# Kernel tuning notes

Measured on AMD Instinct MI355X. Metric: run time of the kernel, lower is better.

The kernel has to match this reference:

```python
import jax, jax.numpy as jnp
import numpy as np

STAGE_SHAPES = {
    'stage1': [(12, 10, 3, 3), (12, 12, 3, 3), (12, 12, 3, 3)],
    'stage2': [(24, 22, 3, 3), (24, 24, 3, 3), (12, 24, 3, 3)],
    'stage3': [(24, 22, 3, 3), (24, 24, 3, 3), (12, 24, 3, 3)],
    'stage4': [(11, 22, 1, 1)],
}
BN_CH = [12, 12, 12, 24, 24, 12, 24, 24, 12]  # channels of the 9 BN layers, in forward order
OFF = np.concatenate([[0], np.cumsum(BN_CH)]).tolist()
EPS = 1e-5


def _split_weights(wflat, shapes):
    """Slice flat [B, P] hypernet weights into per-layer [B, O, I, k, k] tensors."""
    outs, bg = [], 0
    for s in shapes:
        n = int(np.prod(s))
        outs.append(wflat[:, bg:bg + n].reshape((-1,) + s))
        bg += n
    return outs


def _per_sample_conv(x, w):
    """x: [B, C, H, W], w: [B, O, C, k, k] -> [B, O, H, W]. Each sample uses its own filters (SAME padding = k//2 for odd k)."""
    def one(xi, wi):
        return jax.lax.conv_general_dilated(
            xi[None], wi, window_strides=(1, 1), padding='SAME',
            dimension_numbers=('NCHW', 'OIHW', 'NCHW'))[0]
    return jax.vmap(one)(x, w)


def _bn_eval(y, gamma, beta, mean, var):
    """Eval-mode BatchNorm2d over channel dim of [B, C, H, W]."""
    inv = gamma * jax.lax.rsqrt(var + EPS)
    return y * inv[None, :, None, None] + (beta - mean * inv)[None, :, None, None]


def setup_inputs():
    key = jax.random.key(0)
    ks = jax.random.split(key, 8)
    B, H, W = 64, 128, 128
    x = jax.random.normal(ks[0], (B, 10, H, W), jnp.float32)
    # scale hypernet weights down so 9 stacked convs stay numerically tame
    w_stage1 = jax.random.normal(ks[1], (B, 3672), jnp.float32) * 0.05
    w_stage2 = jax.random.normal(ks[2], (B, 12528), jnp.float32) * 0.05
    w_stage3 = jax.random.normal(ks[3], (B, 12528), jnp.float32) * 0.05
    w_stage4 = jax.random.normal(ks[4], (B, 242), jnp.float32) * 0.05
    n_bn = sum(BN_CH)  # 144
    bn_gamma = jax.random.uniform(ks[5], (n_bn,), jnp.float32, 0.5, 1.5)
    bn_beta = jax.random.normal(ks[6], (n_bn,), jnp.float32) * 0.1
    bn_mean = jnp.zeros((n_bn,), jnp.float32)
    bn_var = jnp.ones((n_bn,), jnp.float32)
    return dict(x=x, w_stage1=w_stage1, w_stage2=w_stage2, w_stage3=w_stage3,
                w_stage4=w_stage4, bn_gamma=bn_gamma, bn_beta=bn_beta,
                bn_mean=bn_mean, bn_var=bn_var)


def reference(x, w_stage1, w_stage2, w_stage3, w_stage4, bn_gamma, bn_beta, bn_mean, bn_var):
    cur = x
    li = 0  # global BN layer index
    for stage_key, wflat in (('stage1', w_stage1), ('stage2', w_stage2), ('stage3', w_stage3)):
        for w in _split_weights(wflat, STAGE_SHAPES[stage_key]):
            conv = _per_sample_conv(cur, w)
            lo, hi = OFF[li], OFF[li + 1]
            bn = _bn_eval(conv, bn_gamma[lo:hi], bn_beta[lo:hi], bn_mean[lo:hi], bn_var[lo:hi])
            cur = jax.nn.relu(bn)
            li += 1
        cur = jnp.concatenate([cur, x], axis=1)  # dense skip: [B, 12+10, H, W]
    w_pred = _split_weights(w_stage4, STAGE_SHAPES['stage4'])[0]  # [B, 11, 22, 1, 1]
    return _per_sample_conv(cur, w_pred)
```

## Files before the change

kernel.cpp:

```cpp
#include <hip/hip_runtime.h>
#include <stdint.h>

#define HW    16384
#define NB    64
#define W2    130
#define PXS   (W2*W2)
#define WQH   70144
#define EPSB  1e-5f
#define GP    1444
#define GPB   23104
#define ROWB  608
#define ZPB   2560

typedef _Float16 h8  __attribute__((ext_vector_type(8)));
typedef _Float16 h4  __attribute__((ext_vector_type(4)));
typedef float    f16v __attribute__((ext_vector_type(16)));
typedef float    f4  __attribute__((ext_vector_type(4)));
typedef h8 uh8 __attribute__((aligned(4)));
typedef h4 uh4 __attribute__((aligned(4)));
typedef f4 uf4 __attribute__((aligned(4)));

__global__ void prep_w(const float* __restrict__ w1, const float* __restrict__ w2,
                       const float* __restrict__ w3, const float* __restrict__ w4,
                       const float* __restrict__ g,  const float* __restrict__ be,
                       const float* __restrict__ mu, const float* __restrict__ va,
                       _Float16* __restrict__ wq, float* __restrict__ bias)
{
    const int FO[11]   = {0,576,1152,1728,2880,4032,5184,6336,7488,8640,8768};
    const int start[10]= {0,1080,2376,3672,8424,13608,16200,20952,26136,28728};
    const int COt[10]  = {12,12,12,24,24,12,24,24,12,11};
    const int CIt[10]  = {10,12,12,22,24,24,22,24,24,22};
    const int bnoff[10]= {0,12,24,36,60,84,96,120,144,0};
    const int KST[10]  = {1,1,1,2,2,2,2,2,2,2};

    long tid = (long)blockIdx.x * 256 + threadIdx.x;
    long total = (long)NB * 8768, stride = (long)gridDim.x * 256;
    for (long idx = tid; idx < total; idx += stride) {
        int b = (int)(idx / 8768), i = (int)(idx - (long)b * 8768);
        int l = 9; while (i < FO[l]) --l;
        int j = i - FO[l];
        int f = j >> 6, lane = j & 63;
        int ks = (KST[l] == 2) ? (f & 1) : 0;
        int s  = (KST[l] == 2) ? (f >> 1) : f;
        int co = lane & 31, hi = lane >> 5;
        int CO = COt[l], CI = CIt[l];
        float scale = 1.f;
        if (l < 9 && co < CO) {
            int bi = bnoff[l] + co;
            scale = g[bi] * rsqrtf(va[bi] + EPSB);
        }
        int c0 = ks * 16 + hi * 8;
        __attribute__((aligned(16))) _Float16 vals[8];
#pragma unroll
        for (int e = 0; e < 8; ++e) {
            int c = c0 + e; float wv = 0.f;
            if (co < CO && c < CI) {
                int p = (l < 9) ? start[l] + (co * CI + c) * 9 + s
                                : start[9] + co * CI + c;
                const float* src; long si;
                if      (p <  3672) { src = w1; si = (long)b *  3672 + p; }
                else if (p < 16200) { src = w2; si = (long)b * 12528 + (p -  3672); }
                else if (p < 28728) { src = w3; si = (long)b * 12528 + (p - 16200); }
                else                { src = w4; si = (long)b *   242 + (p - 28728); }
                wv = src[si] * scale;
            }
            vals[e] = (_Float16)wv;
        }
        *(uh8*)(wq + idx * 8) = *(const h8*)vals;
    }
    if (tid < 320) {
        int l = (int)tid >> 5, co = (int)tid & 31;
        float v = 0.f;
        if (l < 9 && co < COt[l]) {
            int bi = bnoff[l] + co;
            float sc = g[bi] * rsqrtf(va[bi] + EPSB);
            v = be[bi] - mu[bi] * sc;
        }
        bias[tid] = v;
    }
}

__global__ void pad_x(const float* __restrict__ x, _Float16* __restrict__ bufA,
                      _Float16* __restrict__ bufB, int b0)
{
    int sl = blockIdx.x >> 3, part = blockIdx.x & 7;
    int gb = b0 + sl;
    const float* __restrict__ xs = x + (long)gb * 10 * HW;
    _Float16* __restrict__ dA = bufA + (long)sl * PXS * 32;
    _Float16* __restrict__ dB = bufB + (long)sl * PXS * 32;
    for (int p = part * 256 + threadIdx.x; p < PXS; p += 2048) {
        int r = p / W2, cc = p - r * W2;
        __attribute__((aligned(16))) _Float16 pxA[32], pxB[32];
#pragma unroll
        for (int i = 0; i < 32; ++i) { pxA[i] = (_Float16)0.f; pxB[i] = (_Float16)0.f; }
        if (r >= 1 && r <= 128 && cc >= 1 && cc <= 128) {
            int so = (r - 1) * 128 + (cc - 1);
#pragma unroll
            for (int c = 0; c < 10; ++c) {
                _Float16 xv = (_Float16)xs[c * HW + so];
                pxA[c] = xv; pxA[12 + c] = xv; pxB[12 + c] = xv;
            }
        }
        _Float16* ap = dA + (long)p * 32;
        _Float16* bp = dB + (long)p * 32;
#pragma unroll
        for (int q = 0; q < 4; ++q) {
            *(uh8*)(ap + q * 8) = *(const h8*)(pxA + q * 8);
            *(uh8*)(bp + q * 8) = *(const h8*)(pxB + q * 8);
        }
    }
}

template<int KST, int NR, int TNWV, bool REV>
__device__ __forceinline__ void lconv(const char* pin, char* pout,
    const char* zbase,
    const _Float16* wl, const float* __restrict__ bias, int boff,
    int rowStart, int nRows, int colStart, int width,
    int oy0, int ox0, int w, int lo5, int hi)
{
    constexpr int qmax = (KST == 1) ? 2 : 3;
    constexpr int NG = 3 * KST;
    constexpr int FR = 9 * KST;

    h8 afr[FR];
#pragma unroll
    for (int f = 0; f < FR; ++f) afr[f] = *(const uh8*)(wl + (long)f * 512);

    const int ncb = (width > 32) ? 2 : 1;
    const int nrg = (nRows + NR - 1) / NR;
    const int nu  = nrg * ncb;
#pragma unroll 1
    for (int u = w; u < nu; u += TNWV) {
        int rg, cb;
        if (ncb == 2) { rg = u >> 1; cb = u & 1; } else { rg = u; cb = 0; }
        int r0 = rowStart + rg * NR;
        { int rmax = rowStart + nRows - NR; r0 = (r0 > rmax) ? rmax : r0; }
        const int cs   = cb ? (colStart + width - 32) : colStart;
        const int cmin = cb ? (64 - width) : 0;
        const char* bin = pin + (long)hi * GPB
                        + ((long)(r0 - 1) * 38 + (cs - 1 + lo5)) * 16;
        const char* binH = bin + 2 * GPB;
        if (KST == 2 && hi) binH = zbase;

        f16v acc[NR];
        { f16v z = {};
#pragma unroll
          for (int i = 0; i < NR; ++i) acc[i] = z; }

#pragma unroll
        for (int gg = 0; gg < NG; ++gg) {
            const int g  = REV ? (NG - 1 - gg) : gg;
            const int kc = g / KST, ks = g - kc * KST;
            const char* base = ks ? binH : bin;
            h8 bf[NR + 2];
#pragma unroll
            for (int j = 0; j < NR + 2; ++j)
                bf[j] = *(const uh8*)(base + kc * 16 + j * ROWB);
            __builtin_amdgcn_s_setprio(1);
#pragma unroll
            for (int kr = 0; kr < 3; ++kr)
#pragma unroll
                for (int tt = 0; tt < NR; ++tt)
                    acc[tt] = __builtin_amdgcn_mfma_f32_32x32x16_f16(
                                  afr[(kr * 3 + kc) * KST + ks], bf[kr + tt], acc[tt], 0, 0, 0);
            __builtin_amdgcn_s_setprio(0);
        }

        f4 bv[qmax];
#pragma unroll
        for (int q = 0; q < qmax; ++q) bv[q] = *(const uf4*)(bias + boff + hi * 4 + q * 8);
        const bool cok = (lo5 >= cmin);
        const int  pc  = cs + lo5;
        const int  gx  = ox0 - 3 + pc;
        const bool xin = (unsigned)(gx - 1) < 128u;
        char* pob = pout + (long)hi * 8 + ((long)r0 * 38 + pc) * 16;
        if (cok) {
#pragma unroll
            for (int tt = 0; tt < NR; ++tt) {
                int gy = oy0 - 3 + r0 + tt;
                bool ok = xin && ((unsigned)(gy - 1) < 128u);
#pragma unroll
                for (int q = 0; q < qmax; ++q) {
                    float v0 = ok ? fmaxf(acc[tt][4*q+0] + bv[q][0], 0.f) : 0.f;
                    float v1 = ok ? fmaxf(acc[tt][4*q+1] + bv[q][1], 0.f) : 0.f;
                    float v2 = ok ? fmaxf(acc[tt][4*q+2] + bv[q][2], 0.f) : 0.f;
                    float v3 = ok ? fmaxf(acc[tt][4*q+3] + bv[q][3], 0.f) : 0.f;
                    h4 hv = { (_Float16)v0, (_Float16)v1, (_Float16)v2, (_Float16)v3 };
                    *(uh4*)(pob + q * GPB + tt * ROWB) = hv;
                }
            }
        }
    }
}

template<int KST, int TNTH>
__global__ __launch_bounds__(TNTH)
void stage3(const _Float16* __restrict__ in, _Float16* __restrict__ out,
            const _Float16* __restrict__ wq, int loff0,
            const float* __restrict__ bias, int boff0, int b0)
{
    constexpr int NGR  = (KST == 1) ? 2 : 3;
    constexpr int PLHk = NGR * GP * 8;
    constexpr int TNWV = TNTH / 64;
    __shared__ _Float16 lds[2][PLHk];
    __shared__ char zpad[(KST == 2) ? ZPB : 16];

    const int t = threadIdx.x, w = t >> 6, l = t & 63;
    const int lo5 = l & 31, hi = l >> 5;

    const int nbb = (int)(gridDim.x >> 4);
    int s, tile;
    if ((nbb & 7) == 0) {
        int xcd = (int)(blockIdx.x & 7), j = (int)(blockIdx.x >> 3);
        s = xcd * (nbb >> 3) + (j >> 4); tile = j & 15;
    } else { s = (int)(blockIdx.x >> 4); tile = (int)(blockIdx.x & 15); }
    const int gb  = b0 + s;
    const int oy0 = 1 + (tile >> 2) * 32;
    const int ox0 = 1 + (tile & 3) * 32;

    {
        constexpr int NLD = NGR * GP;
        constexpr int SI  = (NLD + TNTH - 1) / TNTH;
        const char* src = (const char*)(in + (long)s * PXS * 32);
        char* dst = (char*)&lds[0][0];
        h8 stg[SI];
#pragma unroll
        for (int k = 0; k < SI; ++k) {
            int idx = k * TNTH + t;
            int p = idx / NGR, c = idx - p * NGR;
            int r = p / 38, cc = p - r * 38;
            int gy = oy0 - 3 + r, gx = ox0 - 3 + cc;
            h8 v = {};
            if (idx < NLD && (unsigned)gy < 130u && (unsigned)gx < 130u)
                v = *(const uh8*)(src + ((long)gy * W2 + gx) * 64 + c * 16);
            stg[k] = v;
        }
#pragma unroll
        for (int k = 0; k < SI; ++k) {
            int idx = k * TNTH + t;
            int p = idx / NGR, c = idx - p * NGR;
            if (idx < NLD)
                *(uh8*)(dst + (long)c * GPB + (long)p * 16) = stg[k];
        }
        if (KST == 2 && t < ZPB / 16) {
            h8 z = {};
            *(uh8*)(zpad + t * 16) = z;
        }
    }
    __syncthreads();

    const _Float16* wl = wq + (long)gb * WQH + loff0 + (long)l * 8;
    const char* zb = (const char*)zpad;
    constexpr int LSTEP = 9 * KST * 512;
#define LCONV(PIN, POUT, WOFF, BOFF, RS, NRW, CS, WD)                          \
    if (w & 1) lconv<KST,3,TNWV,true >((const char*)(PIN), (char*)(POUT), zb,  \
        wl + (WOFF), bias, boff0 + (BOFF), RS, NRW, CS, WD, oy0, ox0, w, lo5, hi); \
    else       lconv<KST,3,TNWV,false>((const char*)(PIN), (char*)(POUT), zb,  \
        wl + (WOFF), bias, boff0 + (BOFF), RS, NRW, CS, WD, oy0, ox0, w, lo5, hi);

    LCONV(lds[0], lds[1], 0,         0,  1, 36, 1, 36);
    __syncthreads();
    LCONV(lds[1], lds[0], LSTEP,     32, 2, 34, 2, 34);
    __syncthreads();
    LCONV(lds[0], lds[1], 2 * LSTEP, 64, 3, 32, 3, 32);
    __syncthreads();
#undef LCONV

    {
        _Float16* db = out + (long)s * PXS * 32;
        const char* T = (const char*)&lds[1][0];
        constexpr int WB = (1024 + TNTH - 1) / TNTH;
#pragma unroll
        for (int k = 0; k < WB; ++k) {
            int px = k * TNTH + t;
            if (px < 1024) {
                int pr = 3 + (px >> 5), pc = 3 + (px & 31);
                int gy = oy0 + (px >> 5), gx = ox0 + (px & 31);
                const char* sp = T + ((long)pr * 38 + pc) * 16;
                h8 v0 = *(const uh8*)sp;
                h4 v1 = *(const uh4*)(sp + GPB);
                _Float16* dp = db + ((long)gy * W2 + gx) * 32;
                *(uh8*)dp = v0;
                *(uh4*)(dp + 8) = v1;
            }
        }
    }
}

__global__ __launch_bounds__(256, 2)
void conv1(const _Float16* __restrict__ in, float* __restrict__ outF,
           const _Float16* __restrict__ wq, int loff, int b0)
{
    const int s = blockIdx.y, gb = b0 + s;
    const int t = threadIdx.x, w = t >> 6, l = t & 63;
    const int lo5 = l & 31, hi = l >> 5;
    const int cb = blockIdx.x & 3;
    const int y00 = (blockIdx.x >> 2) * 32 + w * 8;
    const int xpix = cb * 32 + lo5;

    const _Float16* wl = wq + (long)gb * WQH + loff + (long)l * 8;
    h8 a0 = *(const uh8*)(wl);
    h8 a1 = *(const uh8*)(wl + 512);
    const _Float16* ib = in + (long)s * PXS * 32;

#pragma unroll 1
    for (int tt = 0; tt < 8; ++tt) {
        int y = y00 + tt;
        const _Float16* bp = ib + ((long)(y + 1) * W2 + xpix + 1) * 32 + hi * 8;
        h8 bA = *(const uh8*)(bp);
        h8 bB = *(const uh8*)(bp + 16);
        f16v acc = {};
        acc = __builtin_amdgcn_mfma_f32_32x32x16_f16(a0, bA, acc, 0, 0, 0);
        acc = __builtin_amdgcn_mfma_f32_32x32x16_f16(a1, bB, acc, 0, 0, 0);
        long px = (long)y * 128 + xpix;
#pragma unroll
        for (int r = 0; r < 16; ++r) {
            int co = (r & 3) + 8 * (r >> 2) + 4 * hi;
            if (co < 11) outF[((long)gb * 11 + co) * HW + px] = acc[r];
        }
    }
}

extern "C" void kernel_launch(void* const* d_in, const int* in_sizes, int n_in,
                              void* d_out, int out_size, void* d_ws, size_t ws_size,
                              hipStream_t stream)
{
    const float *x = (const float*)d_in[0], *w1 = (const float*)d_in[1],
                *w2 = (const float*)d_in[2], *w3 = (const float*)d_in[3],
                *w4 = (const float*)d_in[4], *g  = (const float*)d_in[5],
                *be = (const float*)d_in[6], *mu = (const float*)d_in[7],
                *va = (const float*)d_in[8];
    if (n_in == 9) {
        const float* big801[2] = {nullptr, nullptr}; int n801 = 0;
        const float* bn156[4]  = {nullptr, nullptr, nullptr, nullptr}; int n156 = 0;
        const float *fx = nullptr, *fw1 = nullptr, *fw4 = nullptr;
        for (int i = 0; i < 9; ++i) {
            int sz = in_sizes[i];
            if      (sz == 10485760) fx  = (const float*)d_in[i];
            else if (sz ==   235008) fw1 = (const float*)d_in[i];
            else if (sz ==   801792) { if (n801 < 2) big801[n801++] = (const float*)d_in[i]; }
            else if (sz ==    15488) fw4 = (const float*)d_in[i];
            else if (sz ==      156) { if (n156 < 4) bn156[n156++] = (const float*)d_in[i]; }
        }
        if (fx && fw1 && fw4 && n801 == 2 && n156 == 4) {
            x = fx; w1 = fw1; w2 = big801[0]; w3 = big801[1]; w4 = fw4;
            g = bn156[0]; be = bn156[1]; mu = bn156[2]; va = bn156[3];
        }
    }
    float* out = (float*)d_out;

    const size_t wqB   = (size_t)NB * WQH * 2;
    const size_t biasB = 2048;
    const size_t hdr   = wqB + biasB;
    const size_t perSlot = (size_t)PXS * 128;
    size_t avail = ws_size > hdr ? ws_size - hdr : 0;
    int chunk = (int)(avail / perSlot);
    if (chunk > NB) chunk = NB;
    if (chunk < 1)  chunk = 1;

    _Float16* wq   = (_Float16*)d_ws;
    float*    bias = (float*)((char*)d_ws + wqB);
    _Float16* bufA = (_Float16*)((char*)d_ws + hdr);
    _Float16* bufB = bufA + (size_t)chunk * PXS * 32;

    prep_w<<<2048, 256, 0, stream>>>(w1, w2, w3, w4, g, be, mu, va, wq, bias);

    for (int b0 = 0; b0 < NB; b0 += chunk) {
        int nb = (NB - b0 < chunk) ? (NB - b0) : chunk;
        pad_x<<<nb * 8, 256, 0, stream>>>(x, bufA, bufB, b0);
        int gc = nb * 16;
        dim3 g1(16, nb);
        stage3<1,1024><<<gc, 1024, 0, stream>>>(bufA, bufB, wq,     0, bias,   0, b0);
        stage3<2, 768><<<gc,  768, 0, stream>>>(bufB, bufA, wq, 13824, bias,  96, b0);
        stage3<2, 768><<<gc,  768, 0, stream>>>(bufA, bufB, wq, 41472, bias, 192, b0);
        conv1<<<g1, 256, 0, stream>>>(bufB, out, wq, 69120, b0);
    }
}
```

Measured before the change: 461.1 us.

## Reshape fused-stage tiles from 32x32 to 16x64 and drop reversed-order waves

Changes the per-block output tile of the fused three-conv stage kernel from 32x32 to 16 rows by 64 columns, widening the LDS halo layout to 22x70 and generalising column blocking to any number of 32-wide chunks. The wider tile lowers the halo overhead in the column direction, which suits the 32-wide MFMA column blocks, at the cost of more row halo. It also removes the reversed tap-group ordering for odd waves, which had been meant to stagger LDS access across waves. LDS footprint per block grows slightly, which may affect occupancy.

```diff
diff --git a/kernel.cpp b/kernel.cpp
--- a/kernel.cpp
+++ b/kernel.cpp
@@ -7,10 +7,12 @@
 #define PXS   (W2*W2)
 #define WQH   70144
 #define EPSB  1e-5f
-#define GP    1444
-#define GPB   23104
-#define ROWB  608
-#define ZPB   2560
+#define WCOL  70
+#define WROW  22
+#define GP    (WROW*WCOL)
+#define GPB   (GP*16)
+#define ROWB  (WCOL*16)
+#define ZPB   4608
 
 typedef _Float16 h8  __attribute__((ext_vector_type(8)));
 typedef _Float16 h4  __attribute__((ext_vector_type(4)));
@@ -111,7 +113,7 @@
     }
 }
 
-template<int KST, int NR, int TNWV, bool REV>
+template<int KST, int NR, int TNWV>
 __device__ __forceinline__ void lconv(const char* pin, char* pout,
     const char* zbase,
     const _Float16* wl, const float* __restrict__ bias, int boff,
@@ -126,19 +128,19 @@
 #pragma unroll
     for (int f = 0; f < FR; ++f) afr[f] = *(const uh8*)(wl + (long)f * 512);
 
-    const int ncb = (width > 32) ? 2 : 1;
+    const int ncb = (width + 31) >> 5;
     const int nrg = (nRows + NR - 1) / NR;
     const int nu  = nrg * ncb;
 #pragma unroll 1
     for (int u = w; u < nu; u += TNWV) {
-        int rg, cb;
-        if (ncb == 2) { rg = u >> 1; cb = u & 1; } else { rg = u; cb = 0; }
+        const int rg = u / ncb, cb = u - rg * ncb;
         int r0 = rowStart + rg * NR;
         { int rmax = rowStart + nRows - NR; r0 = (r0 > rmax) ? rmax : r0; }
-        const int cs   = cb ? (colStart + width - 32) : colStart;
-        const int cmin = cb ? (64 - width) : 0;
+        const bool last = (cb == ncb - 1);
+        const int cs   = last ? (colStart + width - 32) : (colStart + cb * 32);
+        const int cmin = last ? (ncb * 32 - width) : 0;
         const char* bin = pin + (long)hi * GPB
-                        + ((long)(r0 - 1) * 38 + (cs - 1 + lo5)) * 16;
+                        + ((long)(r0 - 1) * WCOL + (cs - 1 + lo5)) * 16;
         const char* binH = bin + 2 * GPB;
         if (KST == 2 && hi) binH = zbase;
 
@@ -148,8 +150,7 @@
           for (int i = 0; i < NR; ++i) acc[i] = z; }
 
 #pragma unroll
-        for (int gg = 0; gg < NG; ++gg) {
-            const int g  = REV ? (NG - 1 - gg) : gg;
+        for (int g = 0; g < NG; ++g) {
             const int kc = g / KST, ks = g - kc * KST;
             const char* base = ks ? binH : bin;
             h8 bf[NR + 2];
@@ -173,7 +174,7 @@
         const int  pc  = cs + lo5;
         const int  gx  = ox0 - 3 + pc;
         const bool xin = (unsigned)(gx - 1) < 128u;
-        char* pob = pout + (long)hi * 8 + ((long)r0 * 38 + pc) * 16;
+        char* pob = pout + (long)hi * 8 + ((long)r0 * WCOL + pc) * 16;
         if (cok) {
 #pragma unroll
             for (int tt = 0; tt < NR; ++tt) {
@@ -215,8 +216,8 @@
         s = xcd * (nbb >> 3) + (j >> 4); tile = j & 15;
     } else { s = (int)(blockIdx.x >> 4); tile = (int)(blockIdx.x & 15); }
     const int gb  = b0 + s;
-    const int oy0 = 1 + (tile >> 2) * 32;
-    const int ox0 = 1 + (tile & 3) * 32;
+    const int oy0 = 1 + (tile >> 1) * 16;
+    const int ox0 = 1 + (tile & 1) * 64;
 
     {
         constexpr int NLD = NGR * GP;
@@ -228,7 +229,7 @@
         for (int k = 0; k < SI; ++k) {
             int idx = k * TNTH + t;
             int p = idx / NGR, c = idx - p * NGR;
-            int r = p / 38, cc = p - r * 38;
+            int r = p / WCOL, cc = p - r * WCOL;
             int gy = oy0 - 3 + r, gx = ox0 - 3 + cc;
             h8 v = {};
             if (idx < NLD && (unsigned)gy < 130u && (unsigned)gx < 130u)
@@ -252,19 +253,15 @@
     const _Float16* wl = wq + (long)gb * WQH + loff0 + (long)l * 8;
     const char* zb = (const char*)zpad;
     constexpr int LSTEP = 9 * KST * 512;
-#define LCONV(PIN, POUT, WOFF, BOFF, RS, NRW, CS, WD)                          \
-    if (w & 1) lconv<KST,3,TNWV,true >((const char*)(PIN), (char*)(POUT), zb,  \
-        wl + (WOFF), bias, boff0 + (BOFF), RS, NRW, CS, WD, oy0, ox0, w, lo5, hi); \
-    else       lconv<KST,3,TNWV,false>((const char*)(PIN), (char*)(POUT), zb,  \
-        wl + (WOFF), bias, boff0 + (BOFF), RS, NRW, CS, WD, oy0, ox0, w, lo5, hi);
-
-    LCONV(lds[0], lds[1], 0,         0,  1, 36, 1, 36);
+    lconv<KST,3,TNWV>((const char*)lds[0], (char*)lds[1], zb, wl,
+                      bias, boff0,      1, 20, 1, 68, oy0, ox0, w, lo5, hi);
     __syncthreads();
-    LCONV(lds[1], lds[0], LSTEP,     32, 2, 34, 2, 34);
+    lconv<KST,3,TNWV>((const char*)lds[1], (char*)lds[0], zb, wl + LSTEP,
+                      bias, boff0 + 32, 2, 18, 2, 66, oy0, ox0, w, lo5, hi);
     __syncthreads();
-    LCONV(lds[0], lds[1], 2 * LSTEP, 64, 3, 32, 3, 32);
+    lconv<KST,3,TNWV>((const char*)lds[0], (char*)lds[1], zb, wl + 2 * LSTEP,
+                      bias, boff0 + 64, 3, 16, 3, 64, oy0, ox0, w, lo5, hi);
     __syncthreads();
-#undef LCONV
 
     {
         _Float16* db = out + (long)s * PXS * 32;
@@ -274,9 +271,9 @@
         for (int k = 0; k < WB; ++k) {
             int px = k * TNTH + t;
             if (px < 1024) {
-                int pr = 3 + (px >> 5), pc = 3 + (px & 31);
-                int gy = oy0 + (px >> 5), gx = ox0 + (px & 31);
-                const char* sp = T + ((long)pr * 38 + pc) * 16;
+                int pr = 3 + (px >> 6), pc = 3 + (px & 63);
+                int gy = oy0 + (px >> 6), gx = ox0 + (px & 63);
+                const char* sp = T + ((long)pr * WCOL + pc) * 16;
                 h8 v0 = *(const uh8*)sp;
                 h4 v1 = *(const uh4*)(sp + GPB);
                 _Float16* dp = db + ((long)gy * W2 + gx) * 32;
```

Result: faster. 439.9 us (-4.6%).
